# Kernel tuning notes

Hardware: AMD Instinct MI355X
Metric: run time of the kernel (lower is better)

The kernel has to match this reference:

```python
import jax, jax.numpy as jnp
import numpy as np

B, S, D_IN, D_OUT, BLK = 2, 2048, 4096, 16384, 32
NBLK = D_IN // BLK  # 128


def setup_inputs() -> dict:
    key = jax.random.key(0)
    k_x, k_q, k_s, k_b = jax.random.split(key, 4)
    x = jax.random.normal(k_x, (B, S, D_IN), dtype=jnp.float32)
    # GGML Q8_0: signed 8-bit quants per block of 32
    qs = jax.random.randint(k_q, (D_OUT, NBLK, BLK), -128, 128, dtype=jnp.int32)
    # per-block scales (stand-in for the fp16 'd' field); small magnitude
    scales = jax.random.uniform(k_s, (D_OUT, NBLK), dtype=jnp.float32) * 0.02
    bias = jax.random.normal(k_b, (D_OUT,), dtype=jnp.float32)
    return {"x": x, "qs": qs, "scales": scales, "bias": bias}


def reference(x, qs, scales, bias):
    # _materialize_weight: block dequantize (d * q per block) then cast to input dtype
    # qs: [O, NBLK, BLK], scales: [O, NBLK] -> W: [O, D_IN]
    W = (scales[:, :, None] * qs.astype(x.dtype)).reshape(D_OUT, D_IN)
    # host Linear: y = x @ W^T + b
    y = jnp.einsum('bsd,od->bso', x, W) + bias
    return y
```

## Files before the change

### kernel.cpp

```cpp
#include <hip/hip_runtime.h>
#include <cstdint>
#include <cstddef>

#define M_DIM 4096
#define N_DIM 16384
#define K_DIM 4096
#define NBLK_Q 128

#define BM 256
#define BN 256
#define BK 64
#define KSTEPS (K_DIM / BK)
#define BUFB 32768
#define NBUF 3

typedef int i32x4 __attribute__((ext_vector_type(4)));
typedef int i32x16 __attribute__((ext_vector_type(16)));

__device__ __forceinline__ void async_copy16(const void* g, void* l) {
  __builtin_amdgcn_global_load_lds((__attribute__((address_space(1))) void*)g,
                                   (__attribute__((address_space(3))) void*)l,
                                   16, 0, 0);
}

#define SFENCE() __builtin_amdgcn_sched_barrier(0)
#define BAR() __builtin_amdgcn_s_barrier()
#define WAITVM(n) asm volatile("s_waitcnt vmcnt(" #n ")")

__global__ __launch_bounds__(256) void quant_x(const float* __restrict__ x,
                                               char* __restrict__ A8S,
                                               float* __restrict__ sxr) {
  const int m = blockIdx.x;
  const int t = threadIdx.x;
  const float* xr = x + (size_t)m * K_DIM + t * 16;
  float4 v[4];
#pragma unroll
  for (int i = 0; i < 4; ++i) v[i] = ((const float4*)xr)[i];
  float amax = 0.f;
#pragma unroll
  for (int i = 0; i < 4; ++i)
    amax = fmaxf(amax, fmaxf(fmaxf(fabsf(v[i].x), fabsf(v[i].y)),
                             fmaxf(fabsf(v[i].z), fabsf(v[i].w))));
#pragma unroll
  for (int off = 32; off; off >>= 1) amax = fmaxf(amax, __shfl_xor(amax, off, 64));
  __shared__ float wmax[4];
  if ((t & 63) == 0) wmax[t >> 6] = amax;
  __syncthreads();
  amax = fmaxf(fmaxf(wmax[0], wmax[1]), fmaxf(wmax[2], wmax[3]));
  const float inv = 127.0f / amax;
  if (t == 0) sxr[m] = amax / 127.0f;
  unsigned d[4];
#pragma unroll
  for (int i = 0; i < 4; ++i) {
    int q0 = (int)rintf(v[i].x * inv), q1 = (int)rintf(v[i].y * inv);
    int q2 = (int)rintf(v[i].z * inv), q3 = (int)rintf(v[i].w * inv);
    d[i] = (q0 & 0xff) | ((q1 & 0xff) << 8) | ((q2 & 0xff) << 16) | ((q3 & 0xff) << 24);
  }
  const int k32 = t >> 1, kg = t & 1;
  const int mtile = m >> 8, mm = m & 255, m32 = mm >> 5, r = mm & 31;
  int4* dst = (int4*)(A8S + ((size_t)(mtile * 128 + k32)) * 8192 + m32 * 1024 + kg * 512 + r * 16);
  *dst = make_int4(d[0], d[1], d[2], d[3]);
}

__global__ __launch_bounds__(256) void pack_w8(const int* __restrict__ qs,
                                               const float* __restrict__ scales,
                                               char* __restrict__ B8S,
                                               float* __restrict__ swc) {
  const int o = blockIdx.x * 4 + (threadIdx.x >> 6);
  const int l = threadIdx.x & 63;
  const float s0 = scales[(size_t)o * NBLK_Q + l];
  const float s1 = scales[(size_t)o * NBLK_Q + 64 + l];
  float S = fmaxf(s0, s1);
#pragma unroll
  for (int off = 32; off; off >>= 1) S = fmaxf(S, __shfl_xor(S, off, 64));
  if (l == 0) swc[o] = S;
  const float rS = 1.0f / S;
  const int nt = o >> 8, col = o & 255, n32 = col >> 5, c = col & 31;
#pragma unroll
  for (int h = 0; h < 2; ++h) {
    const int nb = l + 64 * h;
    const float ratio = ((h == 0) ? s0 : s1) * rS;
    const int4* q = (const int4*)(qs + ((size_t)o * NBLK_Q + nb) * 32);
    unsigned d[8];
#pragma unroll
    for (int g = 0; g < 8; ++g) {
      int4 v = q[g];
      int a0 = (int)rintf((float)v.x * ratio);
      int a1 = (int)rintf((float)v.y * ratio);
      int a2 = (int)rintf((float)v.z * ratio);
      int a3 = (int)rintf((float)v.w * ratio);
      d[g] = (a0 & 0xff) | ((a1 & 0xff) << 8) | ((a2 & 0xff) << 16) | ((a3 & 0xff) << 24);
    }
    char* dst = B8S + ((size_t)(nt * 128 + nb)) * 8192 + n32 * 1024 + c * 16;
    ((int4*)dst)[0] = make_int4(d[0], d[1], d[2], d[3]);
    ((int4*)(dst + 512))[0] = make_int4(d[4], d[5], d[6], d[7]);
  }
}

__global__ __launch_bounds__(512, 2) void gemm_i8(
    const char* __restrict__ A8S, const char* __restrict__ B8S,
    const float* __restrict__ sxr, const float* __restrict__ swc,
    const float* __restrict__ bias, float* __restrict__ C) {
  __shared__ char lds[NBUF * BUFB];

  const int tid = threadIdx.x;
  const int w = tid >> 6;
  const int l = tid & 63;
  const int wm = w >> 2;
  const int wn = w & 3;

  const int bid = blockIdx.x;
  const int wgid = (bid & 7) * 128 + (bid >> 3);
  const int ntile = wgid & 63;
  const int mtile = wgid >> 6;
  const int brow = mtile * BM;
  const int bcol = ntile * BN;

  const char* srcA = A8S + (size_t)mtile * 128 * 8192 + w * 1024 + l * 16;
  const char* srcB = B8S + (size_t)ntile * 128 * 8192 + w * 1024 + l * 16;
  char* const dstA = lds + w * 1024 + l * 16;
  char* const dstB = lds + 8192 + w * 1024 + l * 16;

  auto stage = [&](int q, int buf) {
    q = (q > KSTEPS - 1) ? (KSTEPS - 1) : q;
    const size_t go = (size_t)q * 16384;
    const int bo = buf * BUFB;
    async_copy16(srcA + go, dstA + bo);
    async_copy16(srcA + go + 8192, dstA + bo + 16384);
    async_copy16(srcB + go, dstB + bo);
    async_copy16(srcB + go + 8192, dstB + bo + 16384);
  };

  i32x16 acc[4][2] = {};

  stage(0, 0);
  stage(1, 1);

  for (int kt = 0; kt < KSTEPS; ++kt) {
    WAITVM(4);
    SFENCE(); BAR(); SFENCE();

    const char* bb = lds + (kt % 3) * BUFB;
    i32x4 a[2][4], b[2][2];
#pragma unroll
    for (int s = 0; s < 2; ++s) {
#pragma unroll
      for (int i = 0; i < 4; ++i)
        a[s][i] = *(const i32x4*)(bb + s * 16384 + (wm * 4 + i) * 1024 + l * 16);
#pragma unroll
      for (int j = 0; j < 2; ++j)
        b[s][j] = *(const i32x4*)(bb + s * 16384 + 8192 + (wn * 2 + j) * 1024 + l * 16);
    }

    stage(kt + 2, (kt + 2) % 3);

    __builtin_amdgcn_s_setprio(1);
#pragma unroll
    for (int i = 0; i < 4; ++i)
#pragma unroll
      for (int j = 0; j < 2; ++j) {
        acc[i][j] = __builtin_amdgcn_mfma_i32_32x32x32_i8(a[0][i], b[0][j], acc[i][j], 0, 0, 0);
        acc[i][j] = __builtin_amdgcn_mfma_i32_32x32x32_i8(a[1][i], b[1][j], acc[i][j], 0, 0, 0);
      }
    __builtin_amdgcn_s_setprio(0);
  }

  WAITVM(0);
  SFENCE();

#pragma unroll
  for (int i = 0; i < 4; ++i) {
    const int rb = brow + wm * 128 + i * 32 + 4 * (l >> 5);
#pragma unroll
    for (int j = 0; j < 2; ++j) {
      const int col = bcol + wn * 64 + j * 32 + (l & 31);
      const float Sw = swc[col];
      const float bv = bias[col];
#pragma unroll
      for (int r = 0; r < 16; ++r) {
        const int row = rb + (r & 3) + 8 * (r >> 2);
        C[(size_t)row * N_DIM + col] = (float)acc[i][j][r] * (sxr[row] * Sw) + bv;
      }
    }
  }
}

__global__ void naive_gemm(const float* __restrict__ x, const int* __restrict__ qs,
                           const float* __restrict__ scales, const float* __restrict__ bias,
                           float* __restrict__ y) {
  size_t idx = (size_t)blockIdx.x * 256 + threadIdx.x;
  if (idx >= (size_t)M_DIM * N_DIM) return;
  int o = (int)(idx % N_DIM);
  size_t m = idx / N_DIM;
  const float* xr = x + m * K_DIM;
  const int* q = qs + (size_t)o * K_DIM;
  const float* sc = scales + (size_t)o * NBLK_Q;
  float sum = 0.f;
  for (int nb = 0; nb < NBLK_Q; ++nb) {
    float s = sc[nb];
    float bs = 0.f;
#pragma unroll 8
    for (int b = 0; b < 32; ++b) bs += xr[nb * 32 + b] * (float)q[nb * 32 + b];
    sum += s * bs;
  }
  y[idx] = sum + bias[o];
}

extern "C" void kernel_launch(void* const* d_in, const int* in_sizes, int n_in,
                              void* d_out, int out_size, void* d_ws, size_t ws_size,
                              hipStream_t stream) {
  const float* x = (const float*)d_in[0];
  const int* qs = (const int*)d_in[1];
  const float* scales = (const float*)d_in[2];
  const float* bias = (const float*)d_in[3];
  float* y = (float*)d_out;

  const size_t A8_bytes = (size_t)M_DIM * K_DIM;
  const size_t B8_bytes = (size_t)N_DIM * K_DIM;
  const size_t SX_bytes = (size_t)M_DIM * 4;
  const size_t SW_bytes = (size_t)N_DIM * 4;

  if (ws_size < A8_bytes + B8_bytes + SX_bytes + SW_bytes) {
    size_t total = (size_t)M_DIM * N_DIM;
    naive_gemm<<<(unsigned)((total + 255) / 256), 256, 0, stream>>>(x, qs, scales, bias, y);
    return;
  }

  char* A8S = (char*)d_ws;
  char* B8S = A8S + A8_bytes;
  float* sxr = (float*)(B8S + B8_bytes);
  float* swc = (float*)((char*)sxr + SX_bytes);

  quant_x<<<M_DIM, 256, 0, stream>>>(x, A8S, sxr);
  pack_w8<<<N_DIM / 4, 256, 0, stream>>>(qs, scales, B8S, swc);
  gemm_i8<<<(M_DIM / BM) * (N_DIM / BN), 512, 0, stream>>>(A8S, B8S, sxr, swc, bias, y);
}
```

Measured before the change: 428.6 us.

## Replace async global-to-LDS triple buffering with register-staged double buffering

Drops the direct global_load_lds triple-buffered pipeline and uses a double-buffered scheme instead. Each step loads the next tile into registers, issues the MFMAs, then writes the tile to the other LDS buffer and syncs. The change cuts LDS use from 96KB to 64KB per block, which could help occupancy, and it also remaps block IDs so each XCD covers two M tiles across all N tiles. In exchange it spends VGPRs on staging and adds LDS store instructions, and the prefetch depth drops from two steps to one.

```diff
diff --git a/kernel.cpp b/kernel.cpp
--- a/kernel.cpp
+++ b/kernel.cpp
@@ -12,20 +12,12 @@
 #define BK 64
 #define KSTEPS (K_DIM / BK)
 #define BUFB 32768
-#define NBUF 3
+#define NBUF 2
 
 typedef int i32x4 __attribute__((ext_vector_type(4)));
 typedef int i32x16 __attribute__((ext_vector_type(16)));
 
-__device__ __forceinline__ void async_copy16(const void* g, void* l) {
-  __builtin_amdgcn_global_load_lds((__attribute__((address_space(1))) void*)g,
-                                   (__attribute__((address_space(3))) void*)l,
-                                   16, 0, 0);
-}
-
 #define SFENCE() __builtin_amdgcn_sched_barrier(0)
-#define BAR() __builtin_amdgcn_s_barrier()
-#define WAITVM(n) asm volatile("s_waitcnt vmcnt(" #n ")")
 
 __global__ __launch_bounds__(256) void quant_x(const float* __restrict__ x,
                                                char* __restrict__ A8S,
@@ -101,7 +93,7 @@
     const char* __restrict__ A8S, const char* __restrict__ B8S,
     const float* __restrict__ sxr, const float* __restrict__ swc,
     const float* __restrict__ bias, float* __restrict__ C) {
-  __shared__ char lds[NBUF * BUFB];
+  __shared__ __align__(16) char lds[NBUF * BUFB];
 
   const int tid = threadIdx.x;
   const int w = tid >> 6;
@@ -110,37 +102,34 @@
   const int wn = w & 3;
 
   const int bid = blockIdx.x;
-  const int wgid = (bid & 7) * 128 + (bid >> 3);
-  const int ntile = wgid & 63;
-  const int mtile = wgid >> 6;
+  const int xcd = bid & 7;
+  const int k = bid >> 3;
+  const int mtile = xcd * 2 + (k & 1);
+  const int ntile = k >> 1;
   const int brow = mtile * BM;
   const int bcol = ntile * BN;
 
   const char* srcA = A8S + (size_t)mtile * 128 * 8192 + w * 1024 + l * 16;
   const char* srcB = B8S + (size_t)ntile * 128 * 8192 + w * 1024 + l * 16;
-  char* const dstA = lds + w * 1024 + l * 16;
-  char* const dstB = lds + 8192 + w * 1024 + l * 16;
-
-  auto stage = [&](int q, int buf) {
-    q = (q > KSTEPS - 1) ? (KSTEPS - 1) : q;
-    const size_t go = (size_t)q * 16384;
-    const int bo = buf * BUFB;
-    async_copy16(srcA + go, dstA + bo);
-    async_copy16(srcA + go + 8192, dstA + bo + 16384);
-    async_copy16(srcB + go, dstB + bo);
-    async_copy16(srcB + go + 8192, dstB + bo + 16384);
-  };
+  const int doff = w * 1024 + l * 16;
 
   i32x16 acc[4][2] = {};
 
-  stage(0, 0);
-  stage(1, 1);
+  {
+    int4 ra0 = *(const int4*)(srcA);
+    int4 ra1 = *(const int4*)(srcA + 8192);
+    int4 rb0 = *(const int4*)(srcB);
+    int4 rb1 = *(const int4*)(srcB + 8192);
+    *(int4*)(lds + doff) = ra0;
+    *(int4*)(lds + 16384 + doff) = ra1;
+    *(int4*)(lds + 8192 + doff) = rb0;
+    *(int4*)(lds + 24576 + doff) = rb1;
+    __syncthreads();
+  }
 
   for (int kt = 0; kt < KSTEPS; ++kt) {
-    WAITVM(4);
-    SFENCE(); BAR(); SFENCE();
-
-    const char* bb = lds + (kt % 3) * BUFB;
+    const char* bb = lds + (kt & 1) * BUFB;
+
     i32x4 a[2][4], b[2][2];
 #pragma unroll
     for (int s = 0; s < 2; ++s) {
@@ -152,8 +141,14 @@
         b[s][j] = *(const i32x4*)(bb + s * 16384 + 8192 + (wn * 2 + j) * 1024 + l * 16);
     }
 
-    stage(kt + 2, (kt + 2) % 3);
-
+    const int qn = (kt + 1 > KSTEPS - 1) ? (KSTEPS - 1) : (kt + 1);
+    const size_t go = (size_t)qn * 16384;
+    int4 ra0 = *(const int4*)(srcA + go);
+    int4 ra1 = *(const int4*)(srcA + go + 8192);
+    int4 rb0 = *(const int4*)(srcB + go);
+    int4 rb1 = *(const int4*)(srcB + go + 8192);
+
+    SFENCE();
     __builtin_amdgcn_s_setprio(1);
 #pragma unroll
     for (int i = 0; i < 4; ++i)
@@ -163,10 +158,15 @@
         acc[i][j] = __builtin_amdgcn_mfma_i32_32x32x32_i8(a[1][i], b[1][j], acc[i][j], 0, 0, 0);
       }
     __builtin_amdgcn_s_setprio(0);
-  }
-
-  WAITVM(0);
-  SFENCE();
+    SFENCE();
+
+    char* nb = lds + ((kt + 1) & 1) * BUFB;
+    *(int4*)(nb + doff) = ra0;
+    *(int4*)(nb + 16384 + doff) = ra1;
+    *(int4*)(nb + 8192 + doff) = rb0;
+    *(int4*)(nb + 24576 + doff) = rb1;
+    __syncthreads();
+  }
 
 #pragma unroll
   for (int i = 0; i < 4; ++i) {
```

New measurement: 455.3 us. 6.2% more time.
